# Performance work log

Measured on AMD Instinct MI355X. Metric: run time of the kernel, lower is better.

Reference implementation:

```python
import jax, jax.numpy as jnp
import numpy as np

EPS = 1e-05

def setup_inputs() -> dict:
    key = jax.random.key(0)
    # [bs, r, d] similarity-like matrix, uniform positive entries
    x = jax.random.uniform(key, (16, 2048, 2048), dtype=jnp.float32)
    return {"input": x}

def reference(input) -> jnp.ndarray:
    # Original torch code: D = 1/max(rowsum, EPS); y = diag(D) @ input per batch.
    # Mathematically identical to a row-wise L1 normalization with an EPS clamp.
    row_sum = input.sum(axis=2)                      # [bs, r]
    inv = 1.0 / jnp.maximum(row_sum, EPS)            # [bs, r]
    return input * inv[:, :, None]                   # [bs, r, d]
```

## Files before the change

### kernel.cpp

```cpp
#include <hip/hip_runtime.h>


#define ROW_LEN 2048
#define BLOCK   256

__global__ __launch_bounds__(BLOCK) void rownorm_kernel(
    const float* __restrict__ in, float* __restrict__ out) {
    const int row = blockIdx.x;
    const size_t base = (size_t)row * ROW_LEN;
    const float4* __restrict__ in4 = (const float4*)(in + base);
    float4* __restrict__ out4 = (float4*)(out + base);

    const int t = threadIdx.x;

    float4 a = in4[t];
    float4 b = in4[t + BLOCK];

    float s = (a.x + a.y) + (a.z + a.w) + (b.x + b.y) + (b.z + b.w);

    #pragma unroll
    for (int off = 32; off > 0; off >>= 1)
        s += __shfl_down(s, off, 64);

    __shared__ float wsum[BLOCK / 64];
    __shared__ float inv_s;
    const int lane = t & 63;
    const int wid  = t >> 6;
    if (lane == 0) wsum[wid] = s;
    __syncthreads();
    if (t == 0) {
        float tot = (wsum[0] + wsum[1]) + (wsum[2] + wsum[3]);
        inv_s = 1.0f / fmaxf(tot, 1e-5f);
    }
    __syncthreads();
    const float inv = inv_s;

    a.x *= inv; a.y *= inv; a.z *= inv; a.w *= inv;
    b.x *= inv; b.y *= inv; b.z *= inv; b.w *= inv;
    out4[t]         = a;
    out4[t + BLOCK] = b;
}

extern "C" void kernel_launch(void* const* d_in, const int* in_sizes, int n_in,
                              void* d_out, int out_size, void* d_ws, size_t ws_size,
                              hipStream_t stream) {
    const float* in = (const float*)d_in[0];
    float* out = (float*)d_out;
    const int n_rows = in_sizes[0] / ROW_LEN;
    rownorm_kernel<<<n_rows, BLOCK, 0, stream>>>(in, out);
}
```

Baseline: 425.0 us.

## Map one wavefront per row with nontemporal loads and stores

Each 64-lane wavefront now handles a whole 2048-float row, holding 8 float4 values per lane in registers. The row sum is reduced entirely with xor shuffles, which removes the shared-memory staging and both block barriers. Loads and stores use nontemporal builtins to skip cache retention for this streaming pass. In exchange, each lane uses more registers and each block covers four rows, so there are a quarter as many blocks.

```diff
diff --git a/kernel.cpp b/kernel.cpp
--- a/kernel.cpp
+++ b/kernel.cpp
@@ -1,44 +1,43 @@
 #include <hip/hip_runtime.h>
 
 
+typedef float f32x4 __attribute__((ext_vector_type(4)));
+
 #define ROW_LEN 2048
 #define BLOCK   256
+#define WAVES_PER_BLOCK (BLOCK / 64)
+#define V4_PER_LANE     (ROW_LEN / 4 / 64)
 
 __global__ __launch_bounds__(BLOCK) void rownorm_kernel(
     const float* __restrict__ in, float* __restrict__ out) {
-    const int row = blockIdx.x;
+    const int lane = threadIdx.x & 63;
+    const int wid  = threadIdx.x >> 6;
+    const int row  = blockIdx.x * WAVES_PER_BLOCK + wid;
     const size_t base = (size_t)row * ROW_LEN;
-    const float4* __restrict__ in4 = (const float4*)(in + base);
-    float4* __restrict__ out4 = (float4*)(out + base);
+    const f32x4* __restrict__ in4 = (const f32x4*)(in + base);
+    f32x4* __restrict__ out4      = (f32x4*)(out + base);
 
-    const int t = threadIdx.x;
+    f32x4 v[V4_PER_LANE];
+    #pragma unroll
+    for (int k = 0; k < V4_PER_LANE; ++k)
+        v[k] = __builtin_nontemporal_load(&in4[lane + 64 * k]);
 
-    float4 a = in4[t];
-    float4 b = in4[t + BLOCK];
-
-    float s = (a.x + a.y) + (a.z + a.w) + (b.x + b.y) + (b.z + b.w);
+    float s = 0.0f;
+    #pragma unroll
+    for (int k = 0; k < V4_PER_LANE; ++k)
+        s += (v[k].x + v[k].y) + (v[k].z + v[k].w);
 
     #pragma unroll
-    for (int off = 32; off > 0; off >>= 1)
-        s += __shfl_down(s, off, 64);
+    for (int off = 1; off < 64; off <<= 1)
+        s += __shfl_xor(s, off, 64);
 
-    __shared__ float wsum[BLOCK / 64];
-    __shared__ float inv_s;
-    const int lane = t & 63;
-    const int wid  = t >> 6;
-    if (lane == 0) wsum[wid] = s;
-    __syncthreads();
-    if (t == 0) {
-        float tot = (wsum[0] + wsum[1]) + (wsum[2] + wsum[3]);
-        inv_s = 1.0f / fmaxf(tot, 1e-5f);
+    const float inv = 1.0f / fmaxf(s, 1e-5f);
+
+    #pragma unroll
+    for (int k = 0; k < V4_PER_LANE; ++k) {
+        f32x4 o = v[k] * inv;
+        __builtin_nontemporal_store(o, &out4[lane + 64 * k]);
     }
-    __syncthreads();
-    const float inv = inv_s;
-
-    a.x *= inv; a.y *= inv; a.z *= inv; a.w *= inv;
-    b.x *= inv; b.y *= inv; b.z *= inv; b.w *= inv;
-    out4[t]         = a;
-    out4[t + BLOCK] = b;
 }
 
 extern "C" void kernel_launch(void* const* d_in, const int* in_sizes, int n_in,
@@ -47,5 +46,6 @@
     const float* in = (const float*)d_in[0];
     float* out = (float*)d_out;
     const int n_rows = in_sizes[0] / ROW_LEN;
-    rownorm_kernel<<<n_rows, BLOCK, 0, stream>>>(in, out);
+    const int n_blocks = n_rows / WAVES_PER_BLOCK;
+    rownorm_kernel<<<n_blocks, BLOCK, 0, stream>>>(in, out);
 }
```

After: 420.5 us. Within noise of the previous version (-1.1%).
